# Kernel optimization log

Measured on AMD Instinct MI355X. Metric: run time of the kernel, lower is better.

Reference implementation:

```python
import math
import jax, jax.numpy as jnp
import numpy as np

NUM_BUCKETS = 32
MAX_DISTANCE = 128
N_HEADS = 16
D_KV = 64


def _relative_position_bucket(relative_position, num_buckets=NUM_BUCKETS, max_distance=MAX_DISTANCE):
    # bidirectional (encoder) version, faithful to T5Attention._relative_position_bucket
    nb = num_buckets // 2
    rel_buckets = (relative_position > 0).astype(jnp.int32) * nb
    rp = jnp.abs(relative_position)
    max_exact = nb // 2
    is_small = rp < max_exact
    # log-spaced buckets for large distances; clamp arg of log to >=1 to avoid -inf
    rp_large = max_exact + (
        jnp.log(jnp.maximum(rp, 1).astype(jnp.float32) / max_exact)
        / math.log(max_distance / max_exact)
        * (nb - max_exact)
    ).astype(jnp.int32)
    rp_large = jnp.minimum(rp_large, nb - 1)
    return rel_buckets + jnp.where(is_small, rp, rp_large)


def setup_inputs() -> dict:
    key = jax.random.key(0)
    ks = jax.random.split(key, 6)
    B, S, D = 2, 2048, 1024
    scale = 0.02
    return {
        "hidden_states": jax.random.normal(ks[0], (B, S, D), dtype=jnp.float32),
        "Wq": jax.random.normal(ks[1], (D, N_HEADS * D_KV), dtype=jnp.float32) * scale,
        "Wk": jax.random.normal(ks[2], (D, N_HEADS * D_KV), dtype=jnp.float32) * scale,
        "Wv": jax.random.normal(ks[3], (D, N_HEADS * D_KV), dtype=jnp.float32) * scale,
        "Wo": jax.random.normal(ks[4], (N_HEADS * D_KV, D), dtype=jnp.float32) * scale,
        "rel_bias": jax.random.normal(ks[5], (NUM_BUCKETS, N_HEADS), dtype=jnp.float32),
    }


def reference(hidden_states, Wq, Wk, Wv, Wo, rel_bias):
    B, S, D = hidden_states.shape
    H, dk = N_HEADS, D_KV
    q = (hidden_states @ Wq).reshape(B, S, H, dk)
    k = (hidden_states @ Wk).reshape(B, S, H, dk)
    v = (hidden_states @ Wv).reshape(B, S, H, dk)

    pos = jnp.arange(S)
    relative_position = pos[None, :] - pos[:, None]          # [S_q, S_k]
    buckets = _relative_position_bucket(relative_position)    # [S_q, S_k]
    bias = rel_bias[buckets].transpose(2, 0, 1)               # [H, S_q, S_k]

    # T5 attention: NO 1/sqrt(d) scaling
    scores = jnp.einsum('bqhd,bkhd->bhqk', q, k) + bias[None]
    attn = jax.nn.softmax(scores, axis=-1)
    ctx = jnp.einsum('bhqk,bkhd->bqhd', attn, v).reshape(B, S, H * dk)
    return ctx @ Wo
```

## Files before the change

### kernel.cpp

```cpp
#include <hip/hip_runtime.h>
#include <hip/hip_bf16.h>
#include <stdint.h>

#define S_LEN 2048
#define NH 16
#define NB_DELTA (2*S_LEN-1)
#define LOG2E 1.4426950408889634f

typedef __attribute__((ext_vector_type(8))) __bf16 bf16x8;
typedef __attribute__((ext_vector_type(4))) float f32x4;

__device__ __forceinline__ unsigned short f2bf(float f){
    union { float f; unsigned int u; } v; v.f = f;
    unsigned int u = v.u;
    return (unsigned short)((u + 0x7FFFu + ((u >> 16) & 1u)) >> 16);
}
__device__ __forceinline__ float bf2f(unsigned short u){
    union { unsigned int u; float f; } v; v.u = ((unsigned int)u) << 16;
    return v.f;
}
__device__ __forceinline__ unsigned int pkbf(float a, float b){
    __hip_bfloat162 h = __float22bfloat162_rn(float2{a, b});
    unsigned int u;
    __builtin_memcpy(&u, &h, 4);
    return u;
}
#if __has_builtin(__builtin_amdgcn_exp2f)
__device__ __forceinline__ float fexp2(float x){ return __builtin_amdgcn_exp2f(x); }
#else
__device__ __forceinline__ float fexp2(float x){ return __expf(x * 0.69314718056f); }
#endif

__device__ __forceinline__ void gload16(const void* g, void* l){
    __builtin_amdgcn_global_load_lds(
        (const __attribute__((address_space(1))) void*)(uintptr_t)g,
        (__attribute__((address_space(3))) void*)(uintptr_t)l, 16, 0, 0);
}

__global__ __launch_bounds__(256) void prep_kernel(
    const float* __restrict__ hs, unsigned short* __restrict__ hsb,
    const float* __restrict__ W0, const float* __restrict__ W1,
    const float* __restrict__ W2, const float* __restrict__ W3,
    unsigned short* __restrict__ D0, unsigned short* __restrict__ D1,
    unsigned short* __restrict__ D2, unsigned short* __restrict__ D3,
    const float* __restrict__ rel_bias, float* __restrict__ biasT){
    if (blockIdx.z == 4) {
        int bi = blockIdx.y * 32 + blockIdx.x;
        for (int it = 0; it < 4; it++) {
            int i = bi * 4096 + it * 1024 + threadIdx.x * 4;
            float4 f = *(const float4*)(hs + i);
            ushort4 o;
            o.x = f2bf(f.x); o.y = f2bf(f.y); o.z = f2bf(f.z); o.w = f2bf(f.w);
            *(ushort4*)(hsb + i) = o;
        }
        if (bi < 16) {
            int t = bi * 256 + threadIdx.x;
            if (t < NB_DELTA) {
                int delta = t - (S_LEN - 1);
                int bucket = (delta > 0) ? 16 : 0;
                int a = delta < 0 ? -delta : delta;
                int b;
                if (a < 8) b = a;
                else {
                    int bl = 33 - __builtin_clz(a * a);
                    b = bl < 15 ? bl : 15;
                }
                bucket += b;
                for (int h = 0; h < NH; h++)
                    biasT[h * NB_DELTA + t] = (rel_bias[bucket * NH + h] - 16.f) * LOG2E;
            }
        }
        return;
    }
    const float* src; unsigned short* dst;
    switch (blockIdx.z) {
        case 0: src = W0; dst = D0; break;
        case 1: src = W1; dst = D1; break;
        case 2: src = W2; dst = D2; break;
        default: src = W3; dst = D3; break;
    }
    __shared__ float tile[32][33];
    int bx = blockIdx.x, by = blockIdx.y;
    int tx = threadIdx.x & 31, ty = threadIdx.x >> 5;
    for (int i = 0; i < 4; i++)
        tile[ty + 8*i][tx] = src[(size_t)(by*32 + ty + 8*i) * 1024 + bx*32 + tx];
    __syncthreads();
    for (int i = 0; i < 4; i++)
        dst[(size_t)(bx*32 + ty + 8*i) * 1024 + by*32 + tx] = f2bf(tile[tx][ty + 8*i]);
}

template<int MODE, int BM>
__global__ __launch_bounds__(256) void gemm_bt_kernel(const unsigned short* __restrict__ A,
                                                      const unsigned short* __restrict__ BT,
                                                      float* __restrict__ C0,
                                                      unsigned short* __restrict__ C1,
                                                      unsigned short* __restrict__ Vt,
                                                      const float* __restrict__ RS,
                                                      int Kdim, int ldc){
    constexpr int IT = BM / 32;
    __shared__ __align__(16) unsigned short As[BM * 64];
    __shared__ __align__(16) unsigned short Bs[128 * 64];
    const int t = threadIdx.x;
    const int wave = t >> 6, lane = t & 63;
    const int quad = lane >> 4, l16 = lane & 15;
    const int wm = (wave >> 1) * (BM / 2), wn = (wave & 1) * 64;
    const size_t row0 = (size_t)blockIdx.y * BM, col0 = (size_t)blockIdx.x * 128;

    const int srow8 = lane >> 3;
    const int gg = (lane & 7) ^ srow8;
    const unsigned short* gA = A  + (row0 + wave * 8 + srow8) * (size_t)Kdim + gg * 8;
    const unsigned short* gB = BT + (col0 + wave * 8 + srow8) * (size_t)Kdim + gg * 8;

    f32x4 acc[IT][4] = {};

    bf16x8 pa0[2], pa1[2];
    float ra[2], rb[2];
    auto issueA2 = [&](int kt){
        for (int p = 0; p < 2; p++) {
            size_t row = row0 + p * 32 + wave * 8 + srow8;
            const unsigned short* pp = A + row * 1024 + kt + gg * 8;
            pa0[p] = *(const bf16x8*)pp;
            pa1[p] = *(const bf16x8*)(pp + (size_t)4096 * 1024);
            int head = kt >> 6;
            ra[p] = RS[row * 16 + head];
            rb[p] = RS[(4096 + row) * 16 + head];
        }
    };
    if (MODE == 2) issueA2(0);

    for (int kt = 0; kt < Kdim; kt += 64) {
        if (MODE == 2) {
            for (int p = 0; p < 2; p++) {
                float inv = 1.f / (ra[p] + rb[p]);
                unsigned int u4[4];
                for (int e = 0; e < 4; e++) {
                    float x0 = (float)pa0[p][2 * e]     + (float)pa1[p][2 * e];
                    float x1 = (float)pa0[p][2 * e + 1] + (float)pa1[p][2 * e + 1];
                    u4[e] = pkbf(x0 * inv, x1 * inv);
                }
                bf16x8 pv;
                __builtin_memcpy(&pv, u4, 16);
                *(bf16x8*)&As[(p * 32 + wave * 8) * 64 + lane * 8] = pv;
            }
        } else {
            for (int p = 0; p < BM / 32; p++)
                gload16(gA + (size_t)(p * 32) * Kdim + kt, &As[(p * 32 + wave * 8) * 64]);
        }
        for (int p = 0; p < 4; p++)
            gload16(gB + (size_t)(p * 32) * Kdim + kt, &Bs[(p * 32 + wave * 8) * 64]);
        if (MODE == 2 && kt + 64 < Kdim)
            issueA2(kt + 64);
        __syncthreads();
        bf16x8 a[2][IT], b[2][4];
        for (int ks = 0; ks < 2; ks++) {
            for (int i = 0; i < IT; i++)
                a[ks][i] = *(const bf16x8*)(&As[(wm + i*16 + l16) * 64 + (((ks*4 + quad) ^ (l16 & 7)) * 8)]);
            for (int j = 0; j < 4; j++)
                b[ks][j] = *(const bf16x8*)(&Bs[(wn + j*16 + l16) * 64 + (((ks*4 + quad) ^ (l16 & 7)) * 8)]);
        }
        for (int ks = 0; ks < 2; ks++)
            for (int i = 0; i < IT; i++)
                for (int j = 0; j < 4; j++)
                    acc[i][j] = __builtin_amdgcn_mfma_f32_16x16x32_bf16(a[ks][i], b[ks][j], acc[i][j], 0, 0, 0);
        __syncthreads();
    }
    for (int i = 0; i < IT; i++)
        for (int j = 0; j < 4; j++) {
            size_t r0 = row0 + wm + i*16 + quad*4;
            size_t c  = col0 + wn + j*16 + l16;
            if (MODE == 0 || MODE == 2) {
                for (int r = 0; r < 4; r++)
                    C0[(r0 + r) * ldc + c] = acc[i][j][r];
            } else if (c < 2048) {
                float qs = (c < 1024) ? LOG2E : 1.0f;
                for (int r = 0; r < 4; r++)
                    C1[(r0 + r) * ldc + c] = f2bf(acc[i][j][r] * qs);
            } else {
                size_t bb = r0 >> 11, s = r0 & 2047;
                ushort4 o;
                o.x = f2bf(acc[i][j][0]); o.y = f2bf(acc[i][j][1]);
                o.z = f2bf(acc[i][j][2]); o.w = f2bf(acc[i][j][3]);
                *(ushort4*)(Vt + ((bb << 10) + (c - 2048)) * 2048 + s) = o;
            }
        }
}

__global__ __launch_bounds__(512, 4) void flash18_kernel(
    const unsigned short* __restrict__ qkb,
    const unsigned short* __restrict__ vt,
    const float* __restrict__ biasT,
    unsigned short* __restrict__ ctxpb,
    float* __restrict__ rsbuf)
{
    const int lin  = blockIdx.x;
    const int logi = (lin & 7) * 64 + (lin >> 3);
    const int qt = logi & 7, h = (logi >> 3) & 15;
    const int zz = logi >> 7;
    const int b = zz >> 1, ck = zz & 1;
    const int kt0 = ck << 10;
    const int t = threadIdx.x;
    const int w = t >> 6, lane = t & 63, quad = lane >> 4, l16 = lane & 15;
    const int q0 = qt * 256;

    __shared__ __align__(16) unsigned short Ks[2][64 * 64];
    __shared__ __align__(16) unsigned short Vs[2][64 * 64];
    __shared__ __align__(16) float bias4_b[1280 * 4];

    {
        const float* bsrc = biasT + h * NB_DELTA + (kt0 - q0 + 1792);
        for (int u = t; u < 1276; u += 512) {
            float a0 = bsrc[u], a1 = bsrc[u + 1], a2 = bsrc[u + 2], a3 = bsrc[u + 3];
            float4* d = (float4*)&bias4_b[u * 4];
            *d = float4{a0, a1, a2, a3};
        }
    }
    const int srow8 = lane >> 3;
    const int gg = (lane & 7) ^ srow8;
    const int swz = (l16 & 7) * 8;
    const unsigned short* kbase = qkb + (size_t)(b * S_LEN + w * 8 + srow8) * 2048 + 1024 + h * 64 + gg * 8;
    const unsigned short* vbase = vt + (size_t)(b * 1024 + h * 64 + w * 8 + srow8) * 2048 + gg * 8;
    gload16(kbase + (size_t)kt0 * 2048, &Ks[0][(w * 8) * 64]);
    gload16(vbase + kt0,                &Vs[0][(w * 8) * 64]);

    bf16x8 qb[2][2];
    {
        const unsigned short* qbase =
            qkb + (size_t)(b * S_LEN + q0 + w * 32 + l16) * 2048 + h * 64 + quad * 8;
        for (int nt = 0; nt < 2; nt++)
            for (int ks = 0; ks < 2; ks++)
                qb[ks][nt] = *(const bf16x8*)(qbase + (size_t)nt * 16 * 2048 + ks * 32);
    }
    __syncthreads();

    bf16x8 onesA = {};
    if (l16 == 0) {
        const __bf16 one = (__bf16)1.0f;
        for (int e = 0; e < 8; e++) onesA[e] = one;
    }

    f32x4 ctx[4][2] = {};
    f32x4 rsacc[2] = {};
    const int ib0 = 255 + quad * 4 - w * 32 - l16;

    int cur = 0;
    for (int i = 0; i < 16; i++) {
        if (i < 15) {
            int ktn = kt0 + (i + 1) * 64;
            gload16(kbase + (size_t)ktn * 2048, &Ks[cur ^ 1][(w * 8) * 64]);
            gload16(vbase + ktn,                &Vs[cur ^ 1][(w * 8) * 64]);
        }
        const int ibt = ib0 + i * 64;
        uint2 pk[2][4];
        for (int nb = 0; nb < 4; nb++) {
            const int krow = (nb * 16 + l16) * 64;
            bf16x8 ka0 = *(const bf16x8*)&Ks[cur][krow + ((quad * 8) ^ swz)];
            bf16x8 ka1 = *(const bf16x8*)&Ks[cur][krow + (((4 + quad) * 8) ^ swz)];
            f32x4 st0 = *(const f32x4*)&bias4_b[(ibt + nb * 16) * 4];
            f32x4 st1 = *(const f32x4*)&bias4_b[(ibt - 16 + nb * 16) * 4];
            st0 = __builtin_amdgcn_mfma_f32_16x16x32_bf16(ka0, qb[0][0], st0, 0, 0, 0);
            st0 = __builtin_amdgcn_mfma_f32_16x16x32_bf16(ka1, qb[1][0], st0, 0, 0, 0);
            st1 = __builtin_amdgcn_mfma_f32_16x16x32_bf16(ka0, qb[0][1], st1, 0, 0, 0);
            st1 = __builtin_amdgcn_mfma_f32_16x16x32_bf16(ka1, qb[1][1], st1, 0, 0, 0);
            pk[0][nb].x = pkbf(fexp2(st0[0]), fexp2(st0[1]));
            pk[0][nb].y = pkbf(fexp2(st0[2]), fexp2(st0[3]));
            pk[1][nb].x = pkbf(fexp2(st1[0]), fexp2(st1[1]));
            pk[1][nb].y = pkbf(fexp2(st1[2]), fexp2(st1[3]));
        }
        __builtin_amdgcn_s_setprio(1);
        for (int ks = 0; ks < 2; ks++) {
            bf16x8 pbf[2];
            for (int nt = 0; nt < 2; nt++) {
                uint2 x0 = pk[nt][2 * ks], x1 = pk[nt][2 * ks + 1];
                auto sA = __builtin_amdgcn_permlane32_swap(x0.x, x1.x, false, false);
                auto sB = __builtin_amdgcn_permlane16_swap(sA[0], sA[1], false, false);
                auto sC = __builtin_amdgcn_permlane32_swap(x0.y, x1.y, false, false);
                auto sD = __builtin_amdgcn_permlane16_swap(sC[0], sC[1], false, false);
                unsigned int u4[4] = {sB[0], sD[0], sB[1], sD[1]};
                __builtin_memcpy(&pbf[nt], u4, 16);
            }
            rsacc[0] = __builtin_amdgcn_mfma_f32_16x16x32_bf16(onesA, pbf[0], rsacc[0], 0, 0, 0);
            rsacc[1] = __builtin_amdgcn_mfma_f32_16x16x32_bf16(onesA, pbf[1], rsacc[1], 0, 0, 0);
            for (int nd = 0; nd < 4; nd++) {
                bf16x8 va = *(const bf16x8*)&Vs[cur][(nd * 16 + l16) * 64 + (((ks * 4 + quad) * 8) ^ swz)];
                ctx[nd][0] = __builtin_amdgcn_mfma_f32_16x16x32_bf16(va, pbf[0], ctx[nd][0], 0, 0, 0);
                ctx[nd][1] = __builtin_amdgcn_mfma_f32_16x16x32_bf16(va, pbf[1], ctx[nd][1], 0, 0, 0);
            }
        }
        __builtin_amdgcn_s_setprio(0);
        __syncthreads();
        cur ^= 1;
    }
    unsigned short* cp = ctxpb + (size_t)ck * 4096 * 1024;
    for (int nt = 0; nt < 2; nt++) {
        int row = b * S_LEN + q0 + w * 32 + nt * 16 + l16;
        if (quad == 0) rsbuf[((size_t)ck * 4096 + row) * 16 + h] = rsacc[nt][0];
        for (int nd = 0; nd < 4; nd++) {
            uint2 pk2;
            pk2.x = pkbf(ctx[nd][nt][0], ctx[nd][nt][1]);
            pk2.y = pkbf(ctx[nd][nt][2], ctx[nd][nt][3]);
            *(uint2*)&cp[(size_t)row * 1024 + h * 64 + nd * 16 + quad * 4] = pk2;
        }
    }
}

extern "C" void kernel_launch(void* const* d_in, const int* in_sizes, int n_in,
                              void* d_out, int out_size, void* d_ws, size_t ws_size,
                              hipStream_t stream) {
    const float* hs       = (const float*)d_in[0];
    const float* Wq       = (const float*)d_in[1];
    const float* Wk       = (const float*)d_in[2];
    const float* Wv       = (const float*)d_in[3];
    const float* Wo       = (const float*)d_in[4];
    const float* rel_bias = (const float*)d_in[5];
    float* out = (float*)d_out;

    char* ws = (char*)d_ws;
    float* biasT          = (float*)ws;           ws += 262144;
    unsigned short* hsb   = (unsigned short*)ws;  ws += 8388608;
    unsigned short* WT    = (unsigned short*)ws;  ws += 6291456;
    unsigned short* WoT   = (unsigned short*)ws;  ws += 2097152;
    unsigned short* qkb   = (unsigned short*)ws;  ws += 16777216;
    unsigned short* Vtg   = (unsigned short*)ws;  ws += 8388608;
    unsigned short* ctxpb = (unsigned short*)ws;  ws += 16777216;
    float* rsbuf          = (float*)ws;

    prep_kernel<<<dim3(32, 32, 5), 256, 0, stream>>>(
        hs, hsb, Wq, Wk, Wv, Wo,
        WT, WT + 1024 * 1024, WT + 2 * 1024 * 1024, WoT, rel_bias, biasT);

    gemm_bt_kernel<1, 64><<<dim3(24, 64), 256, 0, stream>>>(hsb, WT, nullptr, qkb, Vtg, nullptr, 1024, 2048);
    flash18_kernel<<<dim3(512), 512, 0, stream>>>(qkb, Vtg, biasT, ctxpb, rsbuf);
    gemm_bt_kernel<2, 64><<<dim3(8, 64), 256, 0, stream>>>(ctxpb, WoT, out, nullptr, nullptr, rsbuf, 1024, 1024);
}
```

Measured before the change: 189.9 us.

## Drop split-K attention, normalize in flash kernel, use plain output GEMM

The attention kernel no longer splits the key range into two halves with partial outputs and row sums. Each block now covers 128 queries over the full key length with 256 threads, and softmax normalization happens in the epilogue. This removes the 16MB partial-context buffer, the row-sum buffer and the merge/normalize work in the output-projection GEMM, which becomes a plain bf16 GEMM. The costs are a longer serial key loop per block, less parallelism per block, and bias reads that are now scalar instead of prepacked float4.

Measured after the change: 194.4 us. 1.02x slower.

```diff
diff --git a/kernel.cpp b/kernel.cpp
--- a/kernel.cpp
+++ b/kernel.cpp
@@ -95,7 +95,6 @@
                                                       float* __restrict__ C0,
                                                       unsigned short* __restrict__ C1,
                                                       unsigned short* __restrict__ Vt,
-                                                      const float* __restrict__ RS,
                                                       int Kdim, int ldc){
     constexpr int IT = BM / 32;
     __shared__ __align__(16) unsigned short As[BM * 64];
@@ -113,43 +112,11 @@
 
     f32x4 acc[IT][4] = {};
 
-    bf16x8 pa0[2], pa1[2];
-    float ra[2], rb[2];
-    auto issueA2 = [&](int kt){
-        for (int p = 0; p < 2; p++) {
-            size_t row = row0 + p * 32 + wave * 8 + srow8;
-            const unsigned short* pp = A + row * 1024 + kt + gg * 8;
-            pa0[p] = *(const bf16x8*)pp;
-            pa1[p] = *(const bf16x8*)(pp + (size_t)4096 * 1024);
-            int head = kt >> 6;
-            ra[p] = RS[row * 16 + head];
-            rb[p] = RS[(4096 + row) * 16 + head];
-        }
-    };
-    if (MODE == 2) issueA2(0);
-
     for (int kt = 0; kt < Kdim; kt += 64) {
-        if (MODE == 2) {
-            for (int p = 0; p < 2; p++) {
-                float inv = 1.f / (ra[p] + rb[p]);
-                unsigned int u4[4];
-                for (int e = 0; e < 4; e++) {
-                    float x0 = (float)pa0[p][2 * e]     + (float)pa1[p][2 * e];
-                    float x1 = (float)pa0[p][2 * e + 1] + (float)pa1[p][2 * e + 1];
-                    u4[e] = pkbf(x0 * inv, x1 * inv);
-                }
-                bf16x8 pv;
-                __builtin_memcpy(&pv, u4, 16);
-                *(bf16x8*)&As[(p * 32 + wave * 8) * 64 + lane * 8] = pv;
-            }
-        } else {
-            for (int p = 0; p < BM / 32; p++)
-                gload16(gA + (size_t)(p * 32) * Kdim + kt, &As[(p * 32 + wave * 8) * 64]);
-        }
+        for (int p = 0; p < BM / 32; p++)
+            gload16(gA + (size_t)(p * 32) * Kdim + kt, &As[(p * 32 + wave * 8) * 64]);
         for (int p = 0; p < 4; p++)
             gload16(gB + (size_t)(p * 32) * Kdim + kt, &Bs[(p * 32 + wave * 8) * 64]);
-        if (MODE == 2 && kt + 64 < Kdim)
-            issueA2(kt + 64);
         __syncthreads();
         bf16x8 a[2][IT], b[2][4];
         for (int ks = 0; ks < 2; ks++) {
@@ -168,7 +135,7 @@
         for (int j = 0; j < 4; j++) {
             size_t r0 = row0 + wm + i*16 + quad*4;
             size_t c  = col0 + wn + j*16 + l16;
-            if (MODE == 0 || MODE == 2) {
+            if (MODE == 0) {
                 for (int r = 0; r < 4; r++)
                     C0[(r0 + r) * ldc + c] = acc[i][j][r];
             } else if (c < 2048) {
@@ -185,42 +152,37 @@
         }
 }
 
-__global__ __launch_bounds__(512, 4) void flash18_kernel(
+__global__ __launch_bounds__(256, 2) void flash19_kernel(
     const unsigned short* __restrict__ qkb,
     const unsigned short* __restrict__ vt,
     const float* __restrict__ biasT,
-    unsigned short* __restrict__ ctxpb,
-    float* __restrict__ rsbuf)
+    unsigned short* __restrict__ ctxb)
 {
     const int lin  = blockIdx.x;
     const int logi = (lin & 7) * 64 + (lin >> 3);
-    const int qt = logi & 7, h = (logi >> 3) & 15;
-    const int zz = logi >> 7;
-    const int b = zz >> 1, ck = zz & 1;
-    const int kt0 = ck << 10;
+    const int qt = logi & 15, h = (logi >> 4) & 15;
+    const int b = logi >> 8;
     const int t = threadIdx.x;
     const int w = t >> 6, lane = t & 63, quad = lane >> 4, l16 = lane & 15;
-    const int q0 = qt * 256;
+    const int q0 = qt * 128;
 
     __shared__ __align__(16) unsigned short Ks[2][64 * 64];
     __shared__ __align__(16) unsigned short Vs[2][64 * 64];
-    __shared__ __align__(16) float bias4_b[1280 * 4];
+    __shared__ float bias_b[2304];
 
     {
-        const float* bsrc = biasT + h * NB_DELTA + (kt0 - q0 + 1792);
-        for (int u = t; u < 1276; u += 512) {
-            float a0 = bsrc[u], a1 = bsrc[u + 1], a2 = bsrc[u + 2], a3 = bsrc[u + 3];
-            float4* d = (float4*)&bias4_b[u * 4];
-            *d = float4{a0, a1, a2, a3};
-        }
+        const float* bsrc = biasT + h * NB_DELTA + (1792 - q0);
+        for (int u = 128 + t; u < 2303; u += 256) bias_b[u] = bsrc[u];
     }
     const int srow8 = lane >> 3;
     const int gg = (lane & 7) ^ srow8;
     const int swz = (l16 & 7) * 8;
-    const unsigned short* kbase = qkb + (size_t)(b * S_LEN + w * 8 + srow8) * 2048 + 1024 + h * 64 + gg * 8;
-    const unsigned short* vbase = vt + (size_t)(b * 1024 + h * 64 + w * 8 + srow8) * 2048 + gg * 8;
-    gload16(kbase + (size_t)kt0 * 2048, &Ks[0][(w * 8) * 64]);
-    gload16(vbase + kt0,                &Vs[0][(w * 8) * 64]);
+    const unsigned short* kbase = qkb + (size_t)(b * S_LEN + w * 16 + srow8) * 2048 + 1024 + h * 64 + gg * 8;
+    const unsigned short* vbase = vt + (size_t)(b * 1024 + h * 64 + w * 16 + srow8) * 2048 + gg * 8;
+    gload16(kbase,                     &Ks[0][(w * 16) * 64]);
+    gload16(kbase + (size_t)8 * 2048,  &Ks[0][(w * 16 + 8) * 64]);
+    gload16(vbase,                     &Vs[0][(w * 16) * 64]);
+    gload16(vbase + (size_t)8 * 2048,  &Vs[0][(w * 16 + 8) * 64]);
 
     bf16x8 qb[2][2];
     {
@@ -243,11 +205,13 @@
     const int ib0 = 255 + quad * 4 - w * 32 - l16;
 
     int cur = 0;
-    for (int i = 0; i < 16; i++) {
-        if (i < 15) {
-            int ktn = kt0 + (i + 1) * 64;
-            gload16(kbase + (size_t)ktn * 2048, &Ks[cur ^ 1][(w * 8) * 64]);
-            gload16(vbase + ktn,                &Vs[cur ^ 1][(w * 8) * 64]);
+    for (int i = 0; i < 32; i++) {
+        if (i < 31) {
+            size_t koff = (size_t)(i + 1) * 64 * 2048;
+            gload16(kbase + koff,                    &Ks[cur ^ 1][(w * 16) * 64]);
+            gload16(kbase + koff + (size_t)8 * 2048, &Ks[cur ^ 1][(w * 16 + 8) * 64]);
+            gload16(vbase + (i + 1) * 64,            &Vs[cur ^ 1][(w * 16) * 64]);
+            gload16(vbase + (i + 1) * 64 + (size_t)8 * 2048, &Vs[cur ^ 1][(w * 16 + 8) * 64]);
         }
         const int ibt = ib0 + i * 64;
         uint2 pk[2][4];
@@ -255,8 +219,9 @@
             const int krow = (nb * 16 + l16) * 64;
             bf16x8 ka0 = *(const bf16x8*)&Ks[cur][krow + ((quad * 8) ^ swz)];
             bf16x8 ka1 = *(const bf16x8*)&Ks[cur][krow + (((4 + quad) * 8) ^ swz)];
-            f32x4 st0 = *(const f32x4*)&bias4_b[(ibt + nb * 16) * 4];
-            f32x4 st1 = *(const f32x4*)&bias4_b[(ibt - 16 + nb * 16) * 4];
+            const int i0 = ibt + nb * 16;
+            f32x4 st0 = {bias_b[i0], bias_b[i0 + 1], bias_b[i0 + 2], bias_b[i0 + 3]};
+            f32x4 st1 = {bias_b[i0 - 16], bias_b[i0 - 15], bias_b[i0 - 14], bias_b[i0 - 13]};
             st0 = __builtin_amdgcn_mfma_f32_16x16x32_bf16(ka0, qb[0][0], st0, 0, 0, 0);
             st0 = __builtin_amdgcn_mfma_f32_16x16x32_bf16(ka1, qb[1][0], st0, 0, 0, 0);
             st1 = __builtin_amdgcn_mfma_f32_16x16x32_bf16(ka0, qb[0][1], st1, 0, 0, 0);
@@ -290,15 +255,15 @@
         __syncthreads();
         cur ^= 1;
     }
-    unsigned short* cp = ctxpb + (size_t)ck * 4096 * 1024;
     for (int nt = 0; nt < 2; nt++) {
+        float rs = __shfl(rsacc[nt][0], l16);
+        float inv = 1.f / rs;
         int row = b * S_LEN + q0 + w * 32 + nt * 16 + l16;
-        if (quad == 0) rsbuf[((size_t)ck * 4096 + row) * 16 + h] = rsacc[nt][0];
         for (int nd = 0; nd < 4; nd++) {
             uint2 pk2;
-            pk2.x = pkbf(ctx[nd][nt][0], ctx[nd][nt][1]);
-            pk2.y = pkbf(ctx[nd][nt][2], ctx[nd][nt][3]);
-            *(uint2*)&cp[(size_t)row * 1024 + h * 64 + nd * 16 + quad * 4] = pk2;
+            pk2.x = pkbf(ctx[nd][nt][0] * inv, ctx[nd][nt][1] * inv);
+            pk2.y = pkbf(ctx[nd][nt][2] * inv, ctx[nd][nt][3] * inv);
+            *(uint2*)&ctxb[(size_t)row * 1024 + h * 64 + nd * 16 + quad * 4] = pk2;
         }
     }
 }
@@ -321,14 +286,13 @@
     unsigned short* WoT   = (unsigned short*)ws;  ws += 2097152;
     unsigned short* qkb   = (unsigned short*)ws;  ws += 16777216;
     unsigned short* Vtg   = (unsigned short*)ws;  ws += 8388608;
-    unsigned short* ctxpb = (unsigned short*)ws;  ws += 16777216;
-    float* rsbuf          = (float*)ws;
+    unsigned short* ctxb  = hsb;
 
     prep_kernel<<<dim3(32, 32, 5), 256, 0, stream>>>(
         hs, hsb, Wq, Wk, Wv, Wo,
         WT, WT + 1024 * 1024, WT + 2 * 1024 * 1024, WoT, rel_bias, biasT);
 
-    gemm_bt_kernel<1, 64><<<dim3(24, 64), 256, 0, stream>>>(hsb, WT, nullptr, qkb, Vtg, nullptr, 1024, 2048);
-    flash18_kernel<<<dim3(512), 512, 0, stream>>>(qkb, Vtg, biasT, ctxpb, rsbuf);
-    gemm_bt_kernel<2, 64><<<dim3(8, 64), 256, 0, stream>>>(ctxpb, WoT, out, nullptr, nullptr, rsbuf, 1024, 1024);
-}
+    gemm_bt_kernel<1, 64><<<dim3(24, 64), 256, 0, stream>>>(hsb, WT, nullptr, qkb, Vtg, 1024, 2048);
+    flash19_kernel<<<dim3(512), 256, 0, stream>>>(qkb, Vtg, biasT, ctxb);
+    gemm_bt_kernel<0, 64><<<dim3(8, 64), 256, 0, stream>>>(ctxb, WoT, out, nullptr, nullptr, 1024, 1024);
+}
```

## Replace QKV projection GEMM with 256x256 double-buffered tile kernel

Applied to the files above, without the earlier changes.

Adds a dedicated QKV projection kernel that uses 256x256 output tiles over 512 threads, double-buffered LDS with async global-to-LDS loads, explicit vmcnt waits and s_setprio around MFMA bursts. Each block reuses more data per tile and overlaps the next K-slice load with compute, cutting global traffic and launch count compared with the old 64x128 tiles. The generic GEMM template is reduced to the output-projection mode only. The trade-off is a grid of only 192 blocks, which may underfill the GPU's compute units, and roughly 128KB of LDS per block.

Result: no change. 188.4 us (-0.8%).

```diff
diff --git a/kernel.cpp b/kernel.cpp
--- a/kernel.cpp
+++ b/kernel.cpp
@@ -89,12 +89,85 @@
         dst[(size_t)(bx*32 + ty + 8*i) * 1024 + by*32 + tx] = f2bf(tile[tx][ty + 8*i]);
 }
 
+__global__ __launch_bounds__(512) void gemm256_kernel(
+    const unsigned short* __restrict__ A,
+    const unsigned short* __restrict__ BT,
+    unsigned short* __restrict__ C1,
+    unsigned short* __restrict__ Vt){
+    constexpr int K = 1024, NK = 16;
+    __shared__ __align__(16) unsigned short As[2][256 * 64];
+    __shared__ __align__(16) unsigned short Bs[2][256 * 64];
+    const int t = threadIdx.x;
+    const int wv = t >> 6, lane = t & 63, quad = lane >> 4, l16 = lane & 15;
+    const int wm = wv >> 2, wn = wv & 3;
+    const size_t row0 = (size_t)blockIdx.y * 256, col0 = (size_t)blockIdx.x * 256;
+
+    const int srow8 = lane >> 3;
+    const int gg = (lane & 7) ^ srow8;
+    const unsigned short* gA = A  + (row0 + wv * 8 + srow8) * (size_t)K + gg * 8;
+    const unsigned short* gB = BT + (col0 + wv * 8 + srow8) * (size_t)K + gg * 8;
+
+    f32x4 acc[8][4] = {};
+
+    auto stage2 = [&](int kt, int p, int buf){
+        gload16(gA + (size_t)(p * 64) * K + kt * 64, &As[buf][(p * 64 + wv * 8) * 64]);
+        gload16(gB + (size_t)(p * 64) * K + kt * 64, &Bs[buf][(p * 64 + wv * 8) * 64]);
+    };
+    for (int p = 0; p < 4; p++) stage2(0, p, 0);
+
+    for (int kt = 0; kt < NK; kt++) {
+        const int cur = kt & 1;
+        bf16x8 bfr[2][4];
+#pragma unroll
+        for (int qd = 0; qd < 4; qd++) {
+            if (kt + 1 < NK) stage2(kt + 1, qd, cur ^ 1);
+            if (qd == 0) {
+                if (kt + 1 < NK) asm volatile("s_waitcnt vmcnt(2)" ::: "memory");
+                else             asm volatile("s_waitcnt vmcnt(0)" ::: "memory");
+            }
+            __builtin_amdgcn_s_barrier();
+            bf16x8 afr[2][2];
+            if (qd == 0) {
+                for (int ks = 0; ks < 2; ks++)
+                    for (int j = 0; j < 4; j++)
+                        bfr[ks][j] = *(const bf16x8*)&Bs[cur][(wn * 64 + j * 16 + l16) * 64 + (((ks * 4 + quad) ^ (l16 & 7)) * 8)];
+            }
+            for (int ks = 0; ks < 2; ks++)
+                for (int i = 0; i < 2; i++)
+                    afr[ks][i] = *(const bf16x8*)&As[cur][(wm * 128 + qd * 32 + i * 16 + l16) * 64 + (((ks * 4 + quad) ^ (l16 & 7)) * 8)];
+            __builtin_amdgcn_s_setprio(1);
+            for (int ks = 0; ks < 2; ks++)
+                for (int i = 0; i < 2; i++)
+                    for (int j = 0; j < 4; j++)
+                        acc[qd * 2 + i][j] = __builtin_amdgcn_mfma_f32_16x16x32_bf16(
+                            afr[ks][i], bfr[ks][j], acc[qd * 2 + i][j], 0, 0, 0);
+            __builtin_amdgcn_s_setprio(0);
+            __builtin_amdgcn_s_barrier();
+        }
+    }
+    const bool isV = (col0 >= 2048);
+    const float qs = (col0 < 1024) ? LOG2E : 1.0f;
+    for (int i = 0; i < 8; i++)
+        for (int j = 0; j < 4; j++) {
+            size_t r0 = row0 + wm * 128 + i * 16 + quad * 4;
+            size_t c  = col0 + wn * 64 + j * 16 + l16;
+            if (!isV) {
+                for (int r = 0; r < 4; r++)
+                    C1[(r0 + r) * 2048 + c] = f2bf(acc[i][j][r] * qs);
+            } else {
+                size_t bb = r0 >> 11, s = r0 & 2047;
+                ushort4 o;
+                o.x = f2bf(acc[i][j][0]); o.y = f2bf(acc[i][j][1]);
+                o.z = f2bf(acc[i][j][2]); o.w = f2bf(acc[i][j][3]);
+                *(ushort4*)(Vt + ((bb << 10) + (c - 2048)) * 2048 + s) = o;
+            }
+        }
+}
+
 template<int MODE, int BM>
 __global__ __launch_bounds__(256) void gemm_bt_kernel(const unsigned short* __restrict__ A,
                                                       const unsigned short* __restrict__ BT,
                                                       float* __restrict__ C0,
-                                                      unsigned short* __restrict__ C1,
-                                                      unsigned short* __restrict__ Vt,
                                                       const float* __restrict__ RS,
                                                       int Kdim, int ldc){
     constexpr int IT = BM / 32;
@@ -108,7 +181,6 @@
 
     const int srow8 = lane >> 3;
     const int gg = (lane & 7) ^ srow8;
-    const unsigned short* gA = A  + (row0 + wave * 8 + srow8) * (size_t)Kdim + gg * 8;
     const unsigned short* gB = BT + (col0 + wave * 8 + srow8) * (size_t)Kdim + gg * 8;
 
     f32x4 acc[IT][4] = {};
@@ -126,29 +198,23 @@
             rb[p] = RS[(4096 + row) * 16 + head];
         }
     };
-    if (MODE == 2) issueA2(0);
-
+    issueA2(0);
     for (int kt = 0; kt < Kdim; kt += 64) {
-        if (MODE == 2) {
-            for (int p = 0; p < 2; p++) {
-                float inv = 1.f / (ra[p] + rb[p]);
-                unsigned int u4[4];
-                for (int e = 0; e < 4; e++) {
-                    float x0 = (float)pa0[p][2 * e]     + (float)pa1[p][2 * e];
-                    float x1 = (float)pa0[p][2 * e + 1] + (float)pa1[p][2 * e + 1];
-                    u4[e] = pkbf(x0 * inv, x1 * inv);
-                }
-                bf16x8 pv;
-                __builtin_memcpy(&pv, u4, 16);
-                *(bf16x8*)&As[(p * 32 + wave * 8) * 64 + lane * 8] = pv;
-            }
-        } else {
-            for (int p = 0; p < BM / 32; p++)
-                gload16(gA + (size_t)(p * 32) * Kdim + kt, &As[(p * 32 + wave * 8) * 64]);
+        for (int p = 0; p < 2; p++) {
+            float inv = 1.f / (ra[p] + rb[p]);
+            unsigned int u4[4];
+            for (int e = 0; e < 4; e++) {
+                float x0 = (float)pa0[p][2 * e]     + (float)pa1[p][2 * e];
+                float x1 = (float)pa0[p][2 * e + 1] + (float)pa1[p][2 * e + 1];
+                u4[e] = pkbf(x0 * inv, x1 * inv);
+            }
+            bf16x8 pv;
+            __builtin_memcpy(&pv, u4, 16);
+            *(bf16x8*)&As[(p * 32 + wave * 8) * 64 + lane * 8] = pv;
         }
         for (int p = 0; p < 4; p++)
             gload16(gB + (size_t)(p * 32) * Kdim + kt, &Bs[(p * 32 + wave * 8) * 64]);
-        if (MODE == 2 && kt + 64 < Kdim)
+        if (kt + 64 < Kdim)
             issueA2(kt + 64);
         __syncthreads();
         bf16x8 a[2][IT], b[2][4];
@@ -168,20 +234,8 @@
         for (int j = 0; j < 4; j++) {
             size_t r0 = row0 + wm + i*16 + quad*4;
             size_t c  = col0 + wn + j*16 + l16;
-            if (MODE == 0 || MODE == 2) {
-                for (int r = 0; r < 4; r++)
-                    C0[(r0 + r) * ldc + c] = acc[i][j][r];
-            } else if (c < 2048) {
-                float qs = (c < 1024) ? LOG2E : 1.0f;
-                for (int r = 0; r < 4; r++)
-                    C1[(r0 + r) * ldc + c] = f2bf(acc[i][j][r] * qs);
-            } else {
-                size_t bb = r0 >> 11, s = r0 & 2047;
-                ushort4 o;
-                o.x = f2bf(acc[i][j][0]); o.y = f2bf(acc[i][j][1]);
-                o.z = f2bf(acc[i][j][2]); o.w = f2bf(acc[i][j][3]);
-                *(ushort4*)(Vt + ((bb << 10) + (c - 2048)) * 2048 + s) = o;
-            }
+            for (int r = 0; r < 4; r++)
+                C0[(r0 + r) * ldc + c] = acc[i][j][r];
         }
 }
 
@@ -328,7 +382,7 @@
         hs, hsb, Wq, Wk, Wv, Wo,
         WT, WT + 1024 * 1024, WT + 2 * 1024 * 1024, WoT, rel_bias, biasT);
 
-    gemm_bt_kernel<1, 64><<<dim3(24, 64), 256, 0, stream>>>(hsb, WT, nullptr, qkb, Vtg, nullptr, 1024, 2048);
+    gemm256_kernel<<<dim3(12, 16), 512, 0, stream>>>(hsb, WT, qkb, Vtg);
     flash18_kernel<<<dim3(512), 512, 0, stream>>>(qkb, Vtg, biasT, ctxpb, rsbuf);
-    gemm_bt_kernel<2, 64><<<dim3(8, 64), 256, 0, stream>>>(ctxpb, WoT, out, nullptr, nullptr, rsbuf, 1024, 1024);
-}
+    gemm_bt_kernel<2, 64><<<dim3(8, 64), 256, 0, stream>>>(ctxpb, WoT, out, rsbuf, 1024, 1024);
+}
```
